# Performance work log

Hardware: AMD Instinct MI355X
Metric: run time of the kernel (lower is better)

## Reference

```python
import jax, jax.numpy as jnp
import numpy as np
import math

D_MODEL = 1024
NUM_HEADS = 16
HEAD_DIM = D_MODEL // NUM_HEADS


def setup_inputs() -> dict:
    key = jax.random.key(0)
    ks = jax.random.split(key, 9)
    B, S = 2, 2048
    scale = 1.0 / math.sqrt(D_MODEL)
    x = jax.random.normal(ks[0], (B, S, D_MODEL), dtype=jnp.float32)
    # torch nn.Linear params: weight [out, in], bias [out]
    Wq = jax.random.normal(ks[1], (D_MODEL, D_MODEL), dtype=jnp.float32) * scale
    bq = jax.random.normal(ks[2], (D_MODEL,), dtype=jnp.float32) * scale
    Wk = jax.random.normal(ks[3], (D_MODEL, D_MODEL), dtype=jnp.float32) * scale
    bk = jax.random.normal(ks[4], (D_MODEL,), dtype=jnp.float32) * scale
    Wv = jax.random.normal(ks[5], (D_MODEL, D_MODEL), dtype=jnp.float32) * scale
    bv = jax.random.normal(ks[6], (D_MODEL,), dtype=jnp.float32) * scale
    Wo = jax.random.normal(ks[7], (D_MODEL, D_MODEL), dtype=jnp.float32) * scale
    bo = jax.random.normal(ks[8], (D_MODEL,), dtype=jnp.float32) * scale
    return {"x": x, "Wq": Wq, "bq": bq, "Wk": Wk, "bk": bk,
            "Wv": Wv, "bv": bv, "Wo": Wo, "bo": bo}


def reference(x, Wq, bq, Wk, bk, Wv, bv, Wo, bo):
    B, S, _ = x.shape
    H, Dh = NUM_HEADS, HEAD_DIM

    def proj(W, b):
        # torch Linear: x @ W.T + b -> [B,S,D] -> [B,H,S,Dh]
        y = jnp.einsum('bsd,ed->bse', x, W) + b
        return y.reshape(B, S, H, Dh).transpose(0, 2, 1, 3)

    Q = proj(Wq, bq)
    K = proj(Wk, bk)
    V = proj(Wv, bv)

    # scores [B,H,S,S], causal mask with -inf, then scale by 1/sqrt(head_dim)
    scores = jnp.einsum('bhqd,bhkd->bhqk', Q, K)
    causal = jnp.tril(jnp.ones((S, S), dtype=bool))
    scores = jnp.where(causal, scores, -jnp.inf)
    A = jax.nn.softmax(scores / math.sqrt(Dh), axis=-1)

    O = jnp.einsum('bhqk,bhkd->bhqd', A, V)  # [B,H,S,Dh]
    O = O.transpose(0, 2, 1, 3).reshape(B, S, H * Dh)
    return jnp.einsum('bsd,ed->bse', O, Wo) + bo
```

## Files before the change

kernel.cpp:

```cpp
#include <hip/hip_runtime.h>


typedef _Float16 f16x8 __attribute__((ext_vector_type(8)));
typedef _Float16 f16x4 __attribute__((ext_vector_type(4)));
typedef _Float16 f16x2 __attribute__((ext_vector_type(2)));
typedef float f32x4 __attribute__((ext_vector_type(4)));

#define S_  2048
#define DM  1024
#define NH  16
#define DH  64

__device__ __forceinline__ void gload_lds16(const void* g, void* s) {
  __builtin_amdgcn_global_load_lds(
      (const __attribute__((address_space(1))) void*)g,
      (__attribute__((address_space(3))) void*)s, 16, 0, 0);
}

__device__ __forceinline__ f16x2 pkrtz(float a, float b) {
  return __builtin_bit_cast(f16x2, __builtin_amdgcn_cvt_pkrtz(a, b));
}


__global__ void cvt_x_kernel(const float* __restrict__ src,
                             _Float16* __restrict__ dst) {
  const int i = blockIdx.x * 256 + threadIdx.x;
  const float4 v = ((const float4*)src)[i];
  f16x4 h;
  h[0] = (_Float16)v.x; h[1] = (_Float16)v.y;
  h[2] = (_Float16)v.z; h[3] = (_Float16)v.w;
  ((f16x4*)dst)[i] = h;
}

__global__ void cvt_w_kernel(const float* __restrict__ w0,
                             const float* __restrict__ w1,
                             const float* __restrict__ w2,
                             const float* __restrict__ w3,
                             _Float16* __restrict__ dst) {
  const int y = blockIdx.y;
  const float* src = (y == 0) ? w0 : (y == 1) ? w1 : (y == 2) ? w2 : w3;
  const int i = blockIdx.x * 256 + threadIdx.x;
  const float4 v = ((const float4*)src)[i];
  f16x4 h;
  h[0] = (_Float16)v.x; h[1] = (_Float16)v.y;
  h[2] = (_Float16)v.z; h[3] = (_Float16)v.w;
  ((f16x4*)(dst + (size_t)y * (DM * DM)))[i] = h;
}

__global__ void bias_fill_kernel(const float* __restrict__ bo,
                                 float* __restrict__ out) {
  const int i = blockIdx.x * 256 + threadIdx.x;
  ((float4*)out)[i] = ((const float4*)bo)[i & 255];
}


__device__ __forceinline__ void gemm_core(
    const _Float16* __restrict__ A, const _Float16* __restrict__ W,
    _Float16* As, _Float16* Ws, f32x4 acc[4][4], int m0, int n0,
    int kbeg, int kend)
{
  const int t = threadIdx.x;
  const int w = t >> 6, l = t & 63;
  const int quad = l >> 4, ln = l & 15;
  const int wm = (w >> 1) << 6, wn = (w & 1) << 6;
  const int srow = l >> 2, scol = (l & 3) << 3;

  for (int k0 = kbeg; k0 < kend; k0 += 32) {
#pragma unroll
    for (int i = 0; i < 2; ++i) {
      const int ra = w * 32 + i * 16;
      gload_lds16(&A[(size_t)(m0 + ra + srow) * DM + k0 + scol], &As[ra * 32]);
      gload_lds16(&W[(size_t)(n0 + ra + srow) * DM + k0 + scol], &Ws[ra * 32]);
    }
    __syncthreads();

    f16x8 af[4], bf[4];
#pragma unroll
    for (int mi = 0; mi < 4; ++mi)
      af[mi] = *(const f16x8*)&As[(wm + mi * 16 + ln) * 32 + quad * 8];
#pragma unroll
    for (int ni = 0; ni < 4; ++ni)
      bf[ni] = *(const f16x8*)&Ws[(wn + ni * 16 + ln) * 32 + quad * 8];
#pragma unroll
    for (int mi = 0; mi < 4; ++mi)
#pragma unroll
      for (int ni = 0; ni < 4; ++ni)
        acc[mi][ni] = __builtin_amdgcn_mfma_f32_16x16x32_f16(
            af[mi], bf[ni], acc[mi][ni], 0, 0, 0);
    __syncthreads();
  }
}

__global__ __launch_bounds__(256, 2) void gemm_qkv_kernel(
    const _Float16* __restrict__ xb, const _Float16* __restrict__ wb,
    const float* __restrict__ bq, const float* __restrict__ bk,
    const float* __restrict__ bv, _Float16* __restrict__ qkv)
{
  __shared__ _Float16 As[128 * 32];
  __shared__ _Float16 Ws[128 * 32];
  const int z = blockIdx.z;
  const _Float16* W = wb + (size_t)z * (DM * DM);
  const float* bias = (z == 0) ? bq : ((z == 1) ? bk : bv);
  _Float16* out = qkv + (size_t)z * 4194304;

  const f32x4 z4 = {0.f, 0.f, 0.f, 0.f};
  f32x4 acc[4][4];
#pragma unroll
  for (int mi = 0; mi < 4; ++mi)
#pragma unroll
    for (int ni = 0; ni < 4; ++ni) acc[mi][ni] = z4;

  const int m0 = blockIdx.y * 128, n0 = blockIdx.x * 128;
  gemm_core(xb, W, As, Ws, acc, m0, n0, 0, DM);

  const int t = threadIdx.x, w = t >> 6, l = t & 63;
  const int quad = l >> 4, ln = l & 15;
  const int wm = (w >> 1) << 6, wn = (w & 1) << 6;
  const float scale = (z == 0) ? 0.18033688f : 1.0f;

#pragma unroll
  for (int ni = 0; ni < 4; ++ni) {
    const int c = n0 + wn + ni * 16 + ln;
    const float bias_c = bias[c];
    const int h = c >> 6, d = c & 63;
#pragma unroll
    for (int mi = 0; mi < 4; ++mi) {
      const int mb = m0 + wm + mi * 16 + quad * 4;
#pragma unroll
      for (int r = 0; r < 4; ++r) {
        const int mg = mb + r;
        const int b = mg >> 11, s = mg & 2047;
        const int bh = b * NH + h;
        const float v = (acc[mi][ni][r] + bias_c) * scale;
        size_t idx;
        if (z == 2)
          idx = (size_t)bh * 131072 + (s >> 5) * 2048 + (d >> 4) * 512 +
                ((s >> 3) & 3) * 128 + (d & 15) * 8 + (s & 7);
        else
          idx = (size_t)bh * 131072 + (s >> 4) * 1024 + (d >> 5) * 512 +
                ((d >> 3) & 3) * 128 + (s & 15) * 8 + (d & 7);
        out[idx] = (_Float16)v;
      }
    }
  }
}

__global__ __launch_bounds__(256, 2) void gemm_out_kernel(
    const _Float16* __restrict__ ob, const _Float16* __restrict__ wo,
    float* __restrict__ out)
{
  __shared__ _Float16 As[128 * 32];
  __shared__ _Float16 Ws[128 * 32];
  const f32x4 z4 = {0.f, 0.f, 0.f, 0.f};
  f32x4 acc[4][4];
#pragma unroll
  for (int mi = 0; mi < 4; ++mi)
#pragma unroll
    for (int ni = 0; ni < 4; ++ni) acc[mi][ni] = z4;

  const int m0 = blockIdx.y * 128, n0 = blockIdx.x * 128;
  const int kbeg = blockIdx.z * 512;
  gemm_core(ob, wo, As, Ws, acc, m0, n0, kbeg, kbeg + 512);

  const int t = threadIdx.x, w = t >> 6, l = t & 63;
  const int quad = l >> 4, ln = l & 15;
  const int wm = (w >> 1) << 6, wn = (w & 1) << 6;

#pragma unroll
  for (int ni = 0; ni < 4; ++ni) {
    const int c = n0 + wn + ni * 16 + ln;
#pragma unroll
    for (int mi = 0; mi < 4; ++mi) {
      const int mb = m0 + wm + mi * 16 + quad * 4;
#pragma unroll
      for (int r = 0; r < 4; ++r)
        atomicAdd(&out[(size_t)(mb + r) * DM + c], acc[mi][ni][r]);
    }
  }
}


template <bool DIAG>
__device__ __forceinline__ void compute_tile(
    const _Float16* __restrict__ kb_, const _Float16* __restrict__ vb_,
    int t, const f16x8 (&qf)[2][2], f32x4 (&oacc)[4][2],
    float (&l_i)[2], _Float16* Ps, int quad, int ln, int l)
{
  f16x8 kf[4], vf[4];
#pragma unroll
  for (int i = 0; i < 4; ++i)
    kf[i] = *(const f16x8*)(kb_ + (size_t)(t * 4 + i) * 512 + l * 8);
#pragma unroll
  for (int i = 0; i < 4; ++i)
    vf[i] = *(const f16x8*)(vb_ + (size_t)(t * 4 + i) * 512 + l * 8);

  const f32x4 z4 = {0.f, 0.f, 0.f, 0.f};
  f32x4 sacc[2][2];
#pragma unroll
  for (int mi = 0; mi < 2; ++mi)
#pragma unroll
    for (int qc = 0; qc < 2; ++qc) sacc[mi][qc] = z4;

#pragma unroll
  for (int ks = 0; ks < 2; ++ks)
#pragma unroll
    for (int mi = 0; mi < 2; ++mi)
#pragma unroll
      for (int qc = 0; qc < 2; ++qc)
        sacc[mi][qc] = __builtin_amdgcn_mfma_f32_16x16x32_f16(
            kf[mi * 2 + ks], qf[qc][ks], sacc[mi][qc], 0, 0, 0);

  const int sw = (ln & 3) << 1;
#pragma unroll
  for (int qc = 0; qc < 2; ++qc) {
    float rs = 0.f;
#pragma unroll
    for (int mi = 0; mi < 2; ++mi) {
      float p[4];
#pragma unroll
      for (int r = 0; r < 4; ++r) {
        p[r] = __builtin_amdgcn_exp2f(sacc[mi][qc][r]);
        if (DIAG && (mi * 16 + quad * 4 + r > qc * 16 + ln)) p[r] = 0.f;
        rs += p[r];
      }
      const f16x2 lo = pkrtz(p[0], p[1]);
      const f16x2 hi = pkrtz(p[2], p[3]);
      const f16x4 pk = __builtin_shufflevector(lo, hi, 0, 1, 2, 3);
      const int g = (mi * 4 + quad) ^ sw;
      *(f16x4*)&Ps[(qc * 16 + ln) * 40 + g * 4] = pk;
    }
    l_i[qc] += rs;
  }

  f16x8 pb[2];
#pragma unroll
  for (int qc = 0; qc < 2; ++qc) {
    const int g2 = (quad * 2) ^ sw;
    pb[qc] = *(const f16x8*)&Ps[(qc * 16 + ln) * 40 + g2 * 4];
  }

#pragma unroll
  for (int di = 0; di < 4; ++di)
#pragma unroll
    for (int qc = 0; qc < 2; ++qc)
      oacc[di][qc] = __builtin_amdgcn_mfma_f32_16x16x32_f16(
          vf[di], pb[qc], oacc[di][qc], 0, 0, 0);
}

__global__ __launch_bounds__(256, 3) void attn_kernel(
    const _Float16* __restrict__ QF, const _Float16* __restrict__ KF,
    const _Float16* __restrict__ VF, _Float16* __restrict__ Ob)
{
  __shared__ _Float16 Ps[4 * 32 * 40];
  __shared__ float mrg[3 * 64 * 34];

  const int i = blockIdx.x;
  const int bh = ((i & 7) << 2) | ((i >> 3) & 3);
  const int p = i >> 5;

  const int tid = threadIdx.x;
  const int w = tid >> 6, l = tid & 63;
  const int quad = l >> 4, ln = l & 15;

  const _Float16* qb_ = QF + (size_t)bh * 131072;
  const _Float16* kb_ = KF + (size_t)bh * 131072;
  const _Float16* vb_ = VF + (size_t)bh * 131072;
  _Float16* psw = Ps + w * (32 * 40);
  const int bidx = bh >> 4, h = bh & 15;

  const f32x4 z4 = {0.f, 0.f, 0.f, 0.f};

#pragma unroll
  for (int mem = 0; mem < 2; ++mem) {
    const int qw = (mem == 0) ? (63 - p) : p;
    const int q0 = qw << 5;

    f16x8 qf[2][2];
#pragma unroll
    for (int qc = 0; qc < 2; ++qc)
#pragma unroll
      for (int ks = 0; ks < 2; ++ks)
        qf[qc][ks] = *(const f16x8*)
            (qb_ + (size_t)((2 * qw + qc) * 2 + ks) * 512 + l * 8);

    f32x4 oacc[4][2];
#pragma unroll
    for (int di = 0; di < 4; ++di)
#pragma unroll
      for (int qc = 0; qc < 2; ++qc) oacc[di][qc] = z4;
    float l_i[2] = {0.f, 0.f};

    int t = w;
    for (; t < qw; t += 4)
      compute_tile<false>(kb_, vb_, t, qf, oacc, l_i, psw, quad, ln, l);
    if (t == qw)
      compute_tile<true>(kb_, vb_, t, qf, oacc, l_i, psw, quad, ln, l);

#pragma unroll
    for (int qc = 0; qc < 2; ++qc) {
      float s = l_i[qc];
      s += __shfl_xor(s, 16);
      s += __shfl_xor(s, 32);
      l_i[qc] = s;
    }

    if (w != 0) {
      float* m_ = &mrg[((w - 1) * 64 + l) * 34];
#pragma unroll
      for (int di = 0; di < 4; ++di)
#pragma unroll
        for (int qc = 0; qc < 2; ++qc)
          *(f32x4*)(m_ + di * 8 + qc * 4) = oacc[di][qc];
      m_[32] = l_i[0];
      m_[33] = l_i[1];
    }
    __syncthreads();
    if (w == 0) {
#pragma unroll
      for (int ww = 0; ww < 3; ++ww) {
        const float* m_ = &mrg[(ww * 64 + l) * 34];
#pragma unroll
        for (int di = 0; di < 4; ++di)
#pragma unroll
          for (int qc = 0; qc < 2; ++qc)
            oacc[di][qc] += *(const f32x4*)(m_ + di * 8 + qc * 4);
        l_i[0] += m_[32];
        l_i[1] += m_[33];
      }
#pragma unroll
      for (int qc = 0; qc < 2; ++qc) {
        const float inv = 1.0f / l_i[qc];
        const int q = q0 + qc * 16 + ln;
        _Float16* orow = Ob + (size_t)(bidx * S_ + q) * DM + h * DH + quad * 4;
#pragma unroll
        for (int di = 0; di < 4; ++di) {
          f16x4 o4;
#pragma unroll
          for (int r = 0; r < 4; ++r)
            o4[r] = (_Float16)(oacc[di][qc][r] * inv);
          *(f16x4*)(orow + di * 16) = o4;
        }
      }
    }
    __syncthreads();
  }
}


extern "C" void kernel_launch(void* const* d_in, const int* in_sizes, int n_in,
                              void* d_out, int out_size, void* d_ws, size_t ws_size,
                              hipStream_t stream) {
  (void)in_sizes; (void)n_in; (void)out_size; (void)ws_size;
  const float* x  = (const float*)d_in[0];
  const float* Wq = (const float*)d_in[1];
  const float* bq = (const float*)d_in[2];
  const float* Wk = (const float*)d_in[3];
  const float* bk = (const float*)d_in[4];
  const float* Wv = (const float*)d_in[5];
  const float* bv = (const float*)d_in[6];
  const float* Wo = (const float*)d_in[7];
  const float* bo = (const float*)d_in[8];

  char* ws = (char*)d_ws;
  _Float16* xb  = (_Float16*)(ws);
  _Float16* wb  = (_Float16*)(ws + (8u << 20));
  _Float16* qkv = (_Float16*)(ws + (16u << 20));
  _Float16* ob  = (_Float16*)(ws + (40u << 20));

  cvt_x_kernel<<<dim3(4096), dim3(256), 0, stream>>>(x, xb);
  cvt_w_kernel<<<dim3(1024, 4), dim3(256), 0, stream>>>(Wq, Wk, Wv, Wo, wb);
  bias_fill_kernel<<<dim3(4096), dim3(256), 0, stream>>>(bo, (float*)d_out);
  gemm_qkv_kernel<<<dim3(8, 32, 3), dim3(256), 0, stream>>>(xb, wb, bq, bk, bv, qkv);
  attn_kernel<<<dim3(1024), dim3(256), 0, stream>>>(
      qkv, qkv + 4194304, qkv + 2 * 4194304, ob);
  gemm_out_kernel<<<dim3(8, 32, 2), dim3(256), 0, stream>>>(
      ob, wb + (size_t)3 * DM * DM, (float*)d_out);
}
```

Measured before the change: 207.3 us.

## Drop split-K atomics in output GEMM, fuse bias, deepen QKV k-step

The output projection GEMM no longer uses split-K with float atomics over a bias-prefilled buffer. It now uses 128x64 tiles over the full K range, adds the bias directly and writes plain stores, which removes the bias_fill launch and the atomic traffic. The QKV GEMM loads two 32-wide K slices per barrier pair, halving the number of syncthreads at the cost of twice the LDS per block. Each output block now walks the whole K range itself, so per-block work grows while the grid count is the same as before.

```diff
diff --git a/kernel.cpp b/kernel.cpp
--- a/kernel.cpp
+++ b/kernel.cpp
@@ -47,75 +47,65 @@
   ((f16x4*)(dst + (size_t)y * (DM * DM)))[i] = h;
 }
 
-__global__ void bias_fill_kernel(const float* __restrict__ bo,
-                                 float* __restrict__ out) {
-  const int i = blockIdx.x * 256 + threadIdx.x;
-  ((float4*)out)[i] = ((const float4*)bo)[i & 255];
-}
-
-
-__device__ __forceinline__ void gemm_core(
-    const _Float16* __restrict__ A, const _Float16* __restrict__ W,
-    _Float16* As, _Float16* Ws, f32x4 acc[4][4], int m0, int n0,
-    int kbeg, int kend)
+
+__global__ __launch_bounds__(256, 2) void gemm_qkv_kernel(
+    const _Float16* __restrict__ xb, const _Float16* __restrict__ wb,
+    const float* __restrict__ bq, const float* __restrict__ bk,
+    const float* __restrict__ bv, _Float16* __restrict__ qkv)
 {
+  __shared__ _Float16 As[2][128 * 32];
+  __shared__ _Float16 Ws[2][128 * 32];
+  const int z = blockIdx.z;
+  const _Float16* W = wb + (size_t)z * (DM * DM);
+  const float* bias = (z == 0) ? bq : ((z == 1) ? bk : bv);
+  _Float16* out = qkv + (size_t)z * 4194304;
+
+  const f32x4 z4 = {0.f, 0.f, 0.f, 0.f};
+  f32x4 acc[4][4];
+#pragma unroll
+  for (int mi = 0; mi < 4; ++mi)
+#pragma unroll
+    for (int ni = 0; ni < 4; ++ni) acc[mi][ni] = z4;
+
+  const int m0 = blockIdx.y * 128, n0 = blockIdx.x * 128;
   const int t = threadIdx.x;
   const int w = t >> 6, l = t & 63;
   const int quad = l >> 4, ln = l & 15;
   const int wm = (w >> 1) << 6, wn = (w & 1) << 6;
   const int srow = l >> 2, scol = (l & 3) << 3;
 
-  for (int k0 = kbeg; k0 < kend; k0 += 32) {
-#pragma unroll
-    for (int i = 0; i < 2; ++i) {
-      const int ra = w * 32 + i * 16;
-      gload_lds16(&A[(size_t)(m0 + ra + srow) * DM + k0 + scol], &As[ra * 32]);
-      gload_lds16(&W[(size_t)(n0 + ra + srow) * DM + k0 + scol], &Ws[ra * 32]);
-    }
-    __syncthreads();
-
-    f16x8 af[4], bf[4];
-#pragma unroll
-    for (int mi = 0; mi < 4; ++mi)
-      af[mi] = *(const f16x8*)&As[(wm + mi * 16 + ln) * 32 + quad * 8];
-#pragma unroll
-    for (int ni = 0; ni < 4; ++ni)
-      bf[ni] = *(const f16x8*)&Ws[(wn + ni * 16 + ln) * 32 + quad * 8];
-#pragma unroll
-    for (int mi = 0; mi < 4; ++mi)
+  for (int k0 = 0; k0 < DM; k0 += 64) {
+#pragma unroll
+    for (int h = 0; h < 2; ++h)
+#pragma unroll
+      for (int i = 0; i < 2; ++i) {
+        const int ra = w * 32 + i * 16;
+        gload_lds16(&xb[(size_t)(m0 + ra + srow) * DM + k0 + h * 32 + scol],
+                    &As[h][ra * 32]);
+        gload_lds16(&W[(size_t)(n0 + ra + srow) * DM + k0 + h * 32 + scol],
+                    &Ws[h][ra * 32]);
+      }
+    __syncthreads();
+
+#pragma unroll
+    for (int h = 0; h < 2; ++h) {
+      f16x8 af[4], bf[4];
+#pragma unroll
+      for (int mi = 0; mi < 4; ++mi)
+        af[mi] = *(const f16x8*)&As[h][(wm + mi * 16 + ln) * 32 + quad * 8];
 #pragma unroll
       for (int ni = 0; ni < 4; ++ni)
-        acc[mi][ni] = __builtin_amdgcn_mfma_f32_16x16x32_f16(
-            af[mi], bf[ni], acc[mi][ni], 0, 0, 0);
-    __syncthreads();
-  }
-}
-
-__global__ __launch_bounds__(256, 2) void gemm_qkv_kernel(
-    const _Float16* __restrict__ xb, const _Float16* __restrict__ wb,
-    const float* __restrict__ bq, const float* __restrict__ bk,
-    const float* __restrict__ bv, _Float16* __restrict__ qkv)
-{
-  __shared__ _Float16 As[128 * 32];
-  __shared__ _Float16 Ws[128 * 32];
-  const int z = blockIdx.z;
-  const _Float16* W = wb + (size_t)z * (DM * DM);
-  const float* bias = (z == 0) ? bq : ((z == 1) ? bk : bv);
-  _Float16* out = qkv + (size_t)z * 4194304;
-
-  const f32x4 z4 = {0.f, 0.f, 0.f, 0.f};
-  f32x4 acc[4][4];
-#pragma unroll
-  for (int mi = 0; mi < 4; ++mi)
-#pragma unroll
-    for (int ni = 0; ni < 4; ++ni) acc[mi][ni] = z4;
-
-  const int m0 = blockIdx.y * 128, n0 = blockIdx.x * 128;
-  gemm_core(xb, W, As, Ws, acc, m0, n0, 0, DM);
-
-  const int t = threadIdx.x, w = t >> 6, l = t & 63;
-  const int quad = l >> 4, ln = l & 15;
-  const int wm = (w >> 1) << 6, wn = (w & 1) << 6;
+        bf[ni] = *(const f16x8*)&Ws[h][(wn + ni * 16 + ln) * 32 + quad * 8];
+#pragma unroll
+      for (int mi = 0; mi < 4; ++mi)
+#pragma unroll
+        for (int ni = 0; ni < 4; ++ni)
+          acc[mi][ni] = __builtin_amdgcn_mfma_f32_16x16x32_f16(
+              af[mi], bf[ni], acc[mi][ni], 0, 0, 0);
+    }
+    __syncthreads();
+  }
+
   const float scale = (z == 0) ? 0.18033688f : 1.0f;
 
 #pragma unroll
@@ -145,36 +135,62 @@
   }
 }
 
+
 __global__ __launch_bounds__(256, 2) void gemm_out_kernel(
     const _Float16* __restrict__ ob, const _Float16* __restrict__ wo,
-    float* __restrict__ out)
+    const float* __restrict__ bo, float* __restrict__ out)
 {
   __shared__ _Float16 As[128 * 32];
-  __shared__ _Float16 Ws[128 * 32];
+  __shared__ _Float16 Ws[64 * 32];
   const f32x4 z4 = {0.f, 0.f, 0.f, 0.f};
-  f32x4 acc[4][4];
-#pragma unroll
-  for (int mi = 0; mi < 4; ++mi)
+  f32x4 acc[2][4];
+#pragma unroll
+  for (int mi = 0; mi < 2; ++mi)
 #pragma unroll
     for (int ni = 0; ni < 4; ++ni) acc[mi][ni] = z4;
 
-  const int m0 = blockIdx.y * 128, n0 = blockIdx.x * 128;
-  const int kbeg = blockIdx.z * 512;
-  gemm_core(ob, wo, As, Ws, acc, m0, n0, kbeg, kbeg + 512);
-
-  const int t = threadIdx.x, w = t >> 6, l = t & 63;
+  const int m0 = blockIdx.y * 128, n0 = blockIdx.x * 64;
+  const int t = threadIdx.x;
+  const int w = t >> 6, l = t & 63;
   const int quad = l >> 4, ln = l & 15;
-  const int wm = (w >> 1) << 6, wn = (w & 1) << 6;
+  const int srow = l >> 2, scol = (l & 3) << 3;
+
+  for (int k0 = 0; k0 < DM; k0 += 32) {
+#pragma unroll
+    for (int i = 0; i < 2; ++i) {
+      const int ra = w * 32 + i * 16;
+      gload_lds16(&ob[(size_t)(m0 + ra + srow) * DM + k0 + scol], &As[ra * 32]);
+    }
+    gload_lds16(&wo[(size_t)(n0 + w * 16 + srow) * DM + k0 + scol],
+                &Ws[w * 16 * 32]);
+    __syncthreads();
+
+    f16x8 af[2], bf[4];
+#pragma unroll
+    for (int mi = 0; mi < 2; ++mi)
+      af[mi] = *(const f16x8*)&As[(w * 32 + mi * 16 + ln) * 32 + quad * 8];
+#pragma unroll
+    for (int ni = 0; ni < 4; ++ni)
+      bf[ni] = *(const f16x8*)&Ws[(ni * 16 + ln) * 32 + quad * 8];
+#pragma unroll
+    for (int mi = 0; mi < 2; ++mi)
+#pragma unroll
+      for (int ni = 0; ni < 4; ++ni)
+        acc[mi][ni] = __builtin_amdgcn_mfma_f32_16x16x32_f16(
+            af[mi], bf[ni], acc[mi][ni], 0, 0, 0);
+    __syncthreads();
+  }
 
 #pragma unroll
   for (int ni = 0; ni < 4; ++ni) {
-    const int c = n0 + wn + ni * 16 + ln;
-#pragma unroll
-    for (int mi = 0; mi < 4; ++mi) {
-      const int mb = m0 + wm + mi * 16 + quad * 4;
+    const int c = n0 + ni * 16 + ln;
+    const float bias_c = bo[c];
+#pragma unroll
+    for (int mi = 0; mi < 2; ++mi) {
+      const int mb = m0 + w * 32 + mi * 16 + quad * 4;
 #pragma unroll
       for (int r = 0; r < 4; ++r)
-        atomicAdd(&out[(size_t)(mb + r) * DM + c], acc[mi][ni][r]);
+        out[(size_t)(mb + r) * DM + c] = acc[mi][ni][r] + bias_c;
     }
   }
 }
@@ -369,10 +385,9 @@
 
   cvt_x_kernel<<<dim3(4096), dim3(256), 0, stream>>>(x, xb);
   cvt_w_kernel<<<dim3(1024, 4), dim3(256), 0, stream>>>(Wq, Wk, Wv, Wo, wb);
-  bias_fill_kernel<<<dim3(4096), dim3(256), 0, stream>>>(bo, (float*)d_out);
   gemm_qkv_kernel<<<dim3(8, 32, 3), dim3(256), 0, stream>>>(xb, wb, bq, bk, bv, qkv);
   attn_kernel<<<dim3(1024), dim3(256), 0, stream>>>(
       qkv, qkv + 4194304, qkv + 2 * 4194304, ob);
-  gemm_out_kernel<<<dim3(8, 32, 2), dim3(256), 0, stream>>>(
-      ob, wb + (size_t)3 * DM * DM, (float*)d_out);
-}
+  gemm_out_kernel<<<dim3(16, 32), dim3(256), 0, stream>>>(
+      ob, wb + (size_t)3 * DM * DM, bo, (float*)d_out);
+}
```

Result: faster. 181.6 us (-12.4%).
